# Kernel tuning notes

Measured on AMD Instinct MI355X. Metric: run time of the kernel, lower is better.

Reference implementation:

```python
import jax, jax.numpy as jnp
import numpy as np

N = 50000
E = 800000
IN_DIM = 16
H = 128
L = 4
EDGE_DIM = 7
LN_EPS = 1e-5


def _linear_params(key, fan_in, fan_out):
    kw, kb = jax.random.split(key)
    w = jax.random.normal(kw, (fan_in, fan_out), jnp.float32) * 0.02
    b = jax.random.normal(kb, (fan_out,), jnp.float32) * 0.02
    return w, b


def setup_inputs() -> dict:
    key = jax.random.key(0)
    ks = jax.random.split(key, 20)
    x = jax.random.normal(ks[0], (N, IN_DIM), jnp.float32)
    pos = jax.random.uniform(ks[1], (N, 3), jnp.float32) * 10.0
    row = jax.random.randint(ks[2], (E,), 0, N, jnp.int32)
    # guarantee no self-loops so distance > 0 (radius_graph uses loop=False)
    off = jax.random.randint(ks[3], (E,), 1, N, jnp.int32)
    col = (row + off) % N
    edge_index = jnp.stack([row, col], axis=0)

    W_in, b_in = _linear_params(ks[4], IN_DIM, H)

    def stack_layers(kbase, fan_in, fan_out):
        ws, bs = [], []
        for l in range(L):
            w, b = _linear_params(jax.random.fold_in(kbase, l), fan_in, fan_out)
            ws.append(w); bs.append(b)
        return jnp.stack(ws), jnp.stack(bs)

    We1, be1 = stack_layers(ks[5], 2 * H + EDGE_DIM, H)
    We2, be2 = stack_layers(ks[6], H, H)
    We3, be3 = stack_layers(ks[7], H, H)
    Wn1, bn1 = stack_layers(ks[8], H + H, H)
    Wn2, bn2 = stack_layers(ks[9], H, H)
    Wn3, bn3 = stack_layers(ks[10], H, H)
    ln_g = jnp.ones((L, H), jnp.float32)
    ln_b = jnp.zeros((L, H), jnp.float32)

    return {
        'x': x, 'pos': pos, 'edge_index': edge_index,
        'W_in': W_in, 'b_in': b_in,
        'We1': We1, 'be1': be1, 'We2': We2, 'be2': be2, 'We3': We3, 'be3': be3,
        'Wn1': Wn1, 'bn1': bn1, 'Wn2': Wn2, 'bn2': bn2, 'Wn3': Wn3, 'bn3': bn3,
        'ln_g': ln_g, 'ln_b': ln_b,
    }


def reference(x, pos, edge_index, W_in, b_in, We1, be1, We2, be2, We3, be3,
              Wn1, bn1, Wn2, bn2, Wn3, bn3, ln_g, ln_b):
    n = x.shape[0]
    row, col = edge_index[0], edge_index[1]  # row=source, col=target (PyG)
    rel_pos = pos[col] - pos[row]                       # (E, 3)
    dist = jnp.linalg.norm(rel_pos, axis=1, keepdims=True)  # (E, 1)
    edge_attr = jnp.concatenate([rel_pos, dist], axis=1)    # (E, 4)

    h = x @ W_in + b_in  # (N, H)
    num_layers = We1.shape[0]
    for l in range(num_layers):
        mom = h[:, 3:6]
        rel_mom = mom[col] - mom[row]                        # (E, 3)
        ea = jnp.concatenate([edge_attr, rel_mom], axis=1)   # (E, 7)
        # PyG: x_i = x[target=col], x_j = x[source=row]; EdgeMLP concats [h_i, h_j, ea]
        m = jnp.concatenate([h[col], h[row], ea], axis=1)    # (E, 2H+7)
        m = jax.nn.relu(m @ We1[l] + be1[l])
        m = jax.nn.relu(m @ We2[l] + be2[l])
        m = m @ We3[l] + be3[l]                              # (E, H)
        agg = jax.ops.segment_sum(m, col, num_segments=n)    # scatter-add to targets
        u = jnp.concatenate([h, agg], axis=1)                # (N, 2H)
        u = jax.nn.relu(u @ Wn1[l] + bn1[l])
        u = jax.nn.relu(u @ Wn2[l] + bn2[l])
        u = u @ Wn3[l] + bn3[l]                              # (N, H)
        h = h + u
        mean = jnp.mean(h, axis=-1, keepdims=True)
        var = jnp.mean(jnp.square(h - mean), axis=-1, keepdims=True)
        h = (h - mean) * jax.lax.rsqrt(var + LN_EPS) * ln_g[l] + ln_b[l]
    return h
```

## Files before the change

kernel.cpp:

```cpp
#include <hip/hip_runtime.h>
#include <stdint.h>

#define NN 50000
#define NE 800000
#define HD 128
#define NL 4
#define NM 64
#define EB 128
#define SCH ((NN + 1023) / 1024)

typedef __bf16 bf16x8 __attribute__((ext_vector_type(8)));
typedef __bf16 bf16x4 __attribute__((ext_vector_type(4)));
typedef float  f32x4  __attribute__((ext_vector_type(4)));

__device__ __forceinline__ f32x4 mfma16(bf16x8 a, bf16x8 b, f32x4 c) {
  return __builtin_amdgcn_mfma_f32_16x16x32_bf16(a, b, c, 0, 0, 0);
}

template<int MT, int NT>
__device__ __forceinline__ void zero_acc(f32x4 (&acc)[MT][NT]) {
#pragma unroll
  for (int i = 0; i < MT; ++i)
#pragma unroll
    for (int j = 0; j < NT; ++j) acc[i][j] = f32x4{0.f, 0.f, 0.f, 0.f};
}

template<int MT, int NT, int KS>
__device__ __forceinline__ void gemm_chunk(const __bf16* A, int sa,
    const __bf16* __restrict__ Bt, int Krow, int k0,
    int m_off, int n_off, int lane, f32x4 (&acc)[MT][NT])
{
  const int arow = lane & 15;
  const int quad = lane >> 4;
  bf16x8 b[KS][NT];
#pragma unroll
  for (int ks = 0; ks < KS; ++ks)
#pragma unroll
    for (int nt = 0; nt < NT; ++nt)
      b[ks][nt] = *reinterpret_cast<const bf16x8*>(
          Bt + (size_t)(n_off + nt * 16 + arow) * Krow + k0 + ks * 32 + quad * 8);
#pragma unroll
  for (int ks = 0; ks < KS; ++ks) {
    const int k = k0 + ks * 32 + quad * 8;
    bf16x8 a[MT];
#pragma unroll
    for (int mt = 0; mt < MT; ++mt)
      a[mt] = *reinterpret_cast<const bf16x8*>(A + (m_off + mt * 16 + arow) * sa + k);
#pragma unroll
    for (int mt = 0; mt < MT; ++mt)
#pragma unroll
      for (int nt = 0; nt < NT; ++nt)
        acc[mt][nt] = mfma16(a[mt], b[ks][nt], acc[mt][nt]);
  }
}

template<int MT, int NT, bool RELU>
__device__ __forceinline__ void store_tile(__bf16* O, int so,
    const float* __restrict__ bias, int m_off, int n_off, int lane,
    f32x4 (&acc)[MT][NT])
{
  const int quad = lane >> 4;
  const int cl = lane & 15;
#pragma unroll
  for (int nt = 0; nt < NT; ++nt) {
    const int col = n_off + nt * 16 + cl;
    const float bv = bias[col];
#pragma unroll
    for (int mt = 0; mt < MT; ++mt)
#pragma unroll
      for (int r = 0; r < 4; ++r) {
        const int row = m_off + mt * 16 + quad * 4 + r;
        float v = acc[mt][nt][r] + bv;
        if (RELU) v = fmaxf(v, 0.f);
        O[row * so + col] = (__bf16)v;
      }
  }
}

__global__ void prep_w(const float* __restrict__ W, __bf16* __restrict__ Wt,
                       int K0, int Kp) {
  int idx = blockIdx.x * 256 + threadIdx.x;
  int total = NL * HD * Kp;
  if (idx >= total) return;
  int l = idx / (HD * Kp);
  int rem = idx - l * HD * Kp;
  int n = rem / Kp;
  int k = rem - n * Kp;
  float v = (k < K0) ? W[((size_t)l * K0 + k) * HD + n] : 0.f;
  Wt[idx] = (__bf16)v;
}

__global__ void prep_pqw(const float* __restrict__ We1,
                         __bf16* __restrict__ Wtopt, __bf16* __restrict__ Wbott) {
  int idx = blockIdx.x * 256 + threadIdx.x;
  if (idx >= NL * HD * HD) return;
  int l = idx / (HD * HD);
  int rem = idx - l * HD * HD;
  int n = rem >> 7;
  int k = rem & 127;
  const float* W = We1 + (size_t)l * 263 * HD;
  float extra = (k >= 3 && k < 6) ? W[(260 + k - 3) * HD + n] : 0.f;
  Wtopt[idx] = (__bf16)(W[k * HD + n] + extra);
  Wbott[idx] = (__bf16)(W[(128 + k) * HD + n] - extra);
}

__global__ void h0_kernel(const float* __restrict__ x, const float* __restrict__ W,
                          const float* __restrict__ b, float* __restrict__ H32,
                          __bf16* __restrict__ HB) {
  int idx = blockIdx.x * 256 + threadIdx.x;
  if (idx >= NN * HD) return;
  int node = idx >> 7, j = idx & 127;
  const float* xr = x + node * 16;
  float s = b[j];
#pragma unroll
  for (int k = 0; k < 16; ++k) s += xr[k] * W[k * HD + j];
  H32[idx] = s;
  HB[idx] = (__bf16)s;
}

__global__ void hist_kernel(const int* __restrict__ ei, int* __restrict__ cnt) {
  int e = blockIdx.x * 256 + threadIdx.x;
  if (e < NE) atomicAdd(&cnt[ei[NE + e]], 1);
}

__global__ void scan_kernel(const int* __restrict__ cnt, int* __restrict__ cur) {
  __shared__ int wsum[16];
  const int t = threadIdx.x;
  const int lane = t & 63, wid = t >> 6;
  const int base = t * SCH;
  int s = 0;
  for (int k = 0; k < SCH; ++k) {
    int i = base + k;
    if (i < NN) s += cnt[i];
  }
  int incl = s;
#pragma unroll
  for (int off = 1; off < 64; off <<= 1) {
    int u = __shfl_up(incl, off, 64);
    if (lane >= off) incl += u;
  }
  if (lane == 63) wsum[wid] = incl;
  __syncthreads();
  int woff = 0;
  for (int k = 0; k < wid; ++k) woff += wsum[k];
  int run = woff + incl - s;
  for (int k = 0; k < SCH; ++k) {
    int i = base + k;
    if (i < NN) { cur[i] = run; run += cnt[i]; }
  }
}

__global__ void scatter_kernel(const int* __restrict__ ei, int* __restrict__ cur,
                               const float* __restrict__ pos,
                               int* __restrict__ ROWS, int* __restrict__ COLS,
                               __bf16* __restrict__ DSTb) {
  int e = blockIdx.x * 256 + threadIdx.x;
  if (e < NE) {
    int r = ei[e], c = ei[NE + e];
    int p = atomicAdd(&cur[c], 1);
    ROWS[p] = r;
    COLS[p] = c;
    float dx = pos[c * 3 + 0] - pos[r * 3 + 0];
    float dy = pos[c * 3 + 1] - pos[r * 3 + 1];
    float dz = pos[c * 3 + 2] - pos[r * 3 + 2];
    DSTb[p] = (__bf16)sqrtf(dx * dx + dy * dy + dz * dz);
  }
}

__global__ __launch_bounds__(256, 4) void pq_kernel(
    const __bf16* __restrict__ HB, const float* __restrict__ pos,
    const __bf16* __restrict__ Wtopt, const __bf16* __restrict__ Wbott,
    const float* __restrict__ W4xyz,
    const float* __restrict__ be1,
    __bf16* __restrict__ PB, __bf16* __restrict__ QB)
{
  __shared__ __bf16 SP[64 * 136];
  __shared__ __bf16 SQ[64 * 136];
  const int t = threadIdx.x;
  const int w = t >> 6, lane = t & 63;
  const int g = w & 1;
  const int half = w >> 1;
  const int base = blockIdx.x * 64;
  const int rbase = base + half * 32;
  const int arow = lane & 15, quad = lane >> 4, cl = lane & 15;

  const __bf16* Wt = g ? Wbott : Wtopt;
  __bf16* S = (g ? SQ : SP) + half * 32 * 136;

  f32x4 acc[2][8];
  zero_acc(acc);
#pragma unroll
  for (int ks = 0; ks < 4; ++ks) {
    const int k = ks * 32 + quad * 8;
    bf16x8 b[8];
#pragma unroll
    for (int nt = 0; nt < 8; ++nt)
      b[nt] = *reinterpret_cast<const bf16x8*>(Wt + (size_t)(nt * 16 + arow) * HD + k);
    bf16x8 a[2];
#pragma unroll
    for (int mt = 0; mt < 2; ++mt) {
      int row = rbase + mt * 16 + arow;
      if (row >= NN) row = NN - 1;
      a[mt] = *reinterpret_cast<const bf16x8*>(HB + (size_t)row * HD + k);
    }
#pragma unroll
    for (int mt = 0; mt < 2; ++mt)
#pragma unroll
      for (int nt = 0; nt < 8; ++nt)
        acc[mt][nt] = mfma16(a[mt], b[nt], acc[mt][nt]);
  }
  float px[2][4], py[2][4], pz[2][4];
#pragma unroll
  for (int mt = 0; mt < 2; ++mt)
#pragma unroll
    for (int r = 0; r < 4; ++r) {
      int row = rbase + mt * 16 + quad * 4 + r;
      if (row >= NN) row = NN - 1;
      px[mt][r] = pos[row * 3 + 0];
      py[mt][r] = pos[row * 3 + 1];
      pz[mt][r] = pos[row * 3 + 2];
    }
#pragma unroll
  for (int nt = 0; nt < 8; ++nt) {
    const int col = nt * 16 + cl;
    const float w0 = W4xyz[col], w1 = W4xyz[HD + col], w2 = W4xyz[2 * HD + col];
    const float bb = g ? 0.f : be1[col];
#pragma unroll
    for (int mt = 0; mt < 2; ++mt)
#pragma unroll
      for (int r = 0; r < 4; ++r) {
        const int row = mt * 16 + quad * 4 + r;
        float dot = px[mt][r] * w0 + py[mt][r] * w1 + pz[mt][r] * w2;
        float v = acc[mt][nt][r] + (g ? -dot : dot) + bb;
        S[row * 136 + col] = (__bf16)v;
      }
  }
  __syncthreads();
#pragma unroll
  for (int u = 0; u < 4; ++u) {
    const int idx = u * 256 + t;
    const int row = idx >> 4, ch = idx & 15;
    const int node = base + row;
    if (node < NN) {
      *reinterpret_cast<uint4*>(PB + (size_t)node * HD + ch * 8) =
          *reinterpret_cast<const uint4*>(SP + row * 136 + ch * 8);
      *reinterpret_cast<uint4*>(QB + (size_t)node * HD + ch * 8) =
          *reinterpret_cast<const uint4*>(SQ + row * 136 + ch * 8);
    }
  }
}

__global__ __launch_bounds__(512, 4) void edge_kernel(
    const __bf16* __restrict__ PB, const __bf16* __restrict__ QB,
    const __bf16* __restrict__ DSTb,
    const int* __restrict__ ROWS, const int* __restrict__ COLS,
    const float* __restrict__ w4d,
    const __bf16* __restrict__ We2t, const __bf16* __restrict__ We3t,
    const float* __restrict__ be2, const float* __restrict__ be3,
    float* __restrict__ AGG)
{
  __shared__ __bf16 S1[EB * 136];
  __shared__ __bf16 S2[EB * 136];
  __shared__ float w4ds[HD], be2s[HD], be3s[HD];
  __shared__ int colS[EB];
  __shared__ unsigned long long bmaskS[EB / 64];
  const int t = threadIdx.x;

  const int nwg = gridDim.x;
  const int q = nwg >> 3, r8 = nwg & 7;
  const int xcd = blockIdx.x & 7, idx8 = blockIdx.x >> 3;
  const int bswz = (xcd < r8 ? xcd * (q + 1) : r8 * (q + 1) + (xcd - r8) * q) + idx8;
  const int base = bswz * EB;

  if (t < HD) { w4ds[t] = w4d[t]; be2s[t] = be2[t]; be3s[t] = be3[t]; }
  if (t < EB) colS[t] = COLS[base + t];
  __syncthreads();

  if (t < EB) {
    int d = (t == EB - 1) || (colS[t + 1] != colS[t]);
    unsigned long long bm = __ballot(d);
    if ((t & 63) == 0) bmaskS[t >> 6] = bm;
  }

  {
    const int i = t >> 2, cg = t & 3;
    const int p = base + i;
    const int c = colS[i];
    const int r = ROWS[p];
    const float dist = (float)DSTb[p];
    const __bf16* Prow = PB + (size_t)c * HD;
    const __bf16* Qrow = QB + (size_t)r * HD;
#pragma unroll
    for (int u = 0; u < 4; ++u) {
      const int ch = cg * 4 + u;
      bf16x8 pv = *reinterpret_cast<const bf16x8*>(Prow + ch * 8);
      bf16x8 qv = *reinterpret_cast<const bf16x8*>(Qrow + ch * 8);
      bf16x8 o;
#pragma unroll
      for (int j = 0; j < 8; ++j) {
        const int col = ch * 8 + j;
        float f = (float)pv[j] + (float)qv[j] + dist * w4ds[col];
        o[j] = (__bf16)fmaxf(f, 0.f);
      }
      *reinterpret_cast<bf16x8*>(S1 + i * 136 + ch * 8) = o;
    }
  }
  __syncthreads();

  const int w = t >> 6, lane = t & 63;
  const int m_off = (w >> 2) * 64, n_off = (w & 3) * 32;
  const int arow = lane & 15, quad = lane >> 4, cl = lane & 15;

  f32x4 acc[4][2];
#pragma unroll
  for (int g = 0; g < 2; ++g) {
    const __bf16* Wt = g ? We3t : We2t;
    const float* bs = g ? be3s : be2s;
    const __bf16* Sin  = g ? S2 : S1;
    __bf16* Sout = g ? S1 : S2;

    bf16x8 b[4][2];
#pragma unroll
    for (int ks = 0; ks < 4; ++ks)
#pragma unroll
      for (int nt = 0; nt < 2; ++nt)
        b[ks][nt] = *reinterpret_cast<const bf16x8*>(
            Wt + (size_t)(n_off + nt * 16 + arow) * HD + ks * 32 + quad * 8);

    zero_acc(acc);
#pragma unroll
    for (int ks = 0; ks < 4; ++ks) {
      const int k = ks * 32 + quad * 8;
      bf16x8 a[4];
#pragma unroll
      for (int mt = 0; mt < 4; ++mt)
        a[mt] = *reinterpret_cast<const bf16x8*>(Sin + (m_off + mt * 16 + arow) * 136 + k);
#pragma unroll
      for (int mt = 0; mt < 4; ++mt)
#pragma unroll
        for (int nt = 0; nt < 2; ++nt)
          acc[mt][nt] = mfma16(a[mt], b[ks][nt], acc[mt][nt]);
    }
#pragma unroll
    for (int nt = 0; nt < 2; ++nt) {
      const int col = n_off + nt * 16 + cl;
      const float bv = bs[col];
#pragma unroll
      for (int mt = 0; mt < 4; ++mt)
#pragma unroll
        for (int r = 0; r < 4; ++r) {
          const int row = m_off + mt * 16 + quad * 4 + r;
          float v = acc[mt][nt][r] + bv;
          if (!g) v = fmaxf(v, 0.f);
          Sout[row * 136 + col] = (__bf16)v;
        }
    }
    __syncthreads();
  }

  {
    const int j = t & 127, qtr = t >> 7;
    const int i0 = qtr * 32;
    unsigned int m = (unsigned int)(bmaskS[qtr >> 1] >> ((qtr & 1) * 32));
    m |= 0x80000000u;
    float s = 0.f;
    for (int r = 0; r < 32; ++r) {
      const int i = i0 + r;
      s += (float)S1[i * 136 + j];
      if ((m >> r) & 1u) {
        atomicAdd(&AGG[(size_t)colS[i] * HD + j], s);
        s = 0.f;
      }
    }
  }
}

__global__ __launch_bounds__(256, 4) void node_kernel(
    const __bf16* __restrict__ HBin, float* __restrict__ AGG,
    const __bf16* __restrict__ Wn1t, const __bf16* __restrict__ Wn2t,
    const __bf16* __restrict__ Wn3t,
    const float* __restrict__ bn1, const float* __restrict__ bn2,
    const float* __restrict__ bn3,
    const float* __restrict__ lng, const float* __restrict__ lnb,
    float* __restrict__ H32, __bf16* __restrict__ HBout,
    float* __restrict__ dout)
{
  __shared__ float SB[NM * 136];
  __shared__ float ps[NM][2], psq[NM][2];
  __shared__ float mean_s[NM], rstd_s[NM];
  __bf16* B16 = reinterpret_cast<__bf16*>(SB);
  const int t = threadIdx.x;
  const int base = blockIdx.x * NM;

  {
    const int i0 = t >> 4, s = t & 15;
#pragma unroll
    for (int g = 0; g < NM / 16; ++g) {
      const int i = g * 16 + i0;
      const int node = base + i;
      uint4 v = make_uint4(0, 0, 0, 0);
      if (node < NN) v = *(reinterpret_cast<const uint4*>(HBin + (size_t)node * HD) + s);
      *reinterpret_cast<uint4*>(&B16[i * 264 + s * 8]) = v;
    }
  }
  for (int idx = t; idx < NM * 32; idx += 256) {
    const int i = idx >> 5, c4 = idx & 31;
    const int node = base + i;
    float4 v = make_float4(0.f, 0.f, 0.f, 0.f);
    if (node < NN) {
      float4* ap = reinterpret_cast<float4*>(AGG + (size_t)node * HD + c4 * 4);
      v = *ap;
      *ap = make_float4(0.f, 0.f, 0.f, 0.f);
    }
    __bf16* d = &B16[i * 264 + HD + c4 * 4];
    d[0] = (__bf16)v.x; d[1] = (__bf16)v.y; d[2] = (__bf16)v.z; d[3] = (__bf16)v.w;
  }
  __syncthreads();

  const int w = t >> 6, lane = t & 63;
  const int m_off = (w >> 1) * 32, n_off = (w & 1) * 64;
  f32x4 acc[2][4];
  __bf16* reg0 = B16;
  __bf16* reg1 = B16 + NM * 136;

  zero_acc(acc);
  gemm_chunk<2, 4, 4>(B16, 264, Wn1t, 256, 0,   m_off, n_off, lane, acc);
  gemm_chunk<2, 4, 4>(B16, 264, Wn1t, 256, 128, m_off, n_off, lane, acc);
  __syncthreads();
  store_tile<2, 4, true>(reg0, 136, bn1, m_off, n_off, lane, acc);
  __syncthreads();
  zero_acc(acc);
  gemm_chunk<2, 4, 4>(reg0, 136, Wn2t, 128, 0, m_off, n_off, lane, acc);
  store_tile<2, 4, true>(reg1, 136, bn2, m_off, n_off, lane, acc);
  __syncthreads();
  zero_acc(acc);
  gemm_chunk<2, 4, 4>(reg1, 136, Wn3t, 128, 0, m_off, n_off, lane, acc);
  __syncthreads();

  {
    const int quad = lane >> 4, cl = lane & 15;
#pragma unroll
    for (int nt = 0; nt < 4; ++nt) {
      const int col = n_off + nt * 16 + cl;
      const float bv = bn3[col];
#pragma unroll
      for (int mt = 0; mt < 2; ++mt)
#pragma unroll
        for (int r = 0; r < 4; ++r) {
          const int row = m_off + mt * 16 + quad * 4 + r;
          const int node = base + row;
          float hv = (node < NN) ? H32[(size_t)node * HD + col] : 0.f;
          SB[row * 136 + col] = hv + acc[mt][nt][r] + bv;
        }
    }
  }
  __syncthreads();
  if (t < 128) {
    const int r = t >> 1, hh = t & 1;
    float s = 0.f, sq = 0.f;
    for (int j = hh * 64; j < hh * 64 + 64; ++j) {
      float v = SB[r * 136 + j];
      s += v; sq += v * v;
    }
    ps[r][hh] = s; psq[r][hh] = sq;
  }
  __syncthreads();
  if (t < NM) {
    float s = ps[t][0] + ps[t][1];
    float sq = psq[t][0] + psq[t][1];
    float mean = s * (1.f / HD);
    float var = sq * (1.f / HD) - mean * mean;
    mean_s[t] = mean;
    rstd_s[t] = rsqrtf(var + 1e-5f);
  }
  __syncthreads();
  for (int idx = t; idx < NM * HD; idx += 256) {
    const int r = idx >> 7, j = idx & 127;
    const int node = base + r;
    if (node < NN) {
      float v = (SB[r * 136 + j] - mean_s[r]) * rstd_s[r] * lng[j] + lnb[j];
      H32[(size_t)node * HD + j] = v;
      HBout[(size_t)node * HD + j] = (__bf16)v;
      if (dout) dout[(size_t)node * HD + j] = v;
    }
  }
}

extern "C" void kernel_launch(void* const* d_in, const int* in_sizes, int n_in,
                              void* d_out, int out_size, void* d_ws, size_t ws_size,
                              hipStream_t stream)
{
  const float* x    = (const float*)d_in[0];
  const float* pos  = (const float*)d_in[1];
  const int*   ei   = (const int*)d_in[2];
  const float* W_in = (const float*)d_in[3];
  const float* b_in = (const float*)d_in[4];
  const float* We1  = (const float*)d_in[5];
  const float* be1  = (const float*)d_in[6];
  const float* We2  = (const float*)d_in[7];
  const float* be2  = (const float*)d_in[8];
  const float* We3  = (const float*)d_in[9];
  const float* be3  = (const float*)d_in[10];
  const float* Wn1  = (const float*)d_in[11];
  const float* bn1  = (const float*)d_in[12];
  const float* Wn2  = (const float*)d_in[13];
  const float* bn2  = (const float*)d_in[14];
  const float* Wn3  = (const float*)d_in[15];
  const float* bn3  = (const float*)d_in[16];
  const float* lng  = (const float*)d_in[17];
  const float* lnb  = (const float*)d_in[18];
  float* out = (float*)d_out;

  char* ws = (char*)d_ws;
  size_t off = 0;
  auto alloc = [&](size_t bytes) -> char* {
    char* p = ws + off;
    off += (bytes + 255) & ~(size_t)255;
    return p;
  };
  __bf16* Wtopt = (__bf16*)alloc((size_t)NL * HD * HD * 2);
  __bf16* Wbott = (__bf16*)alloc((size_t)NL * HD * HD * 2);
  __bf16* We2t = (__bf16*)alloc((size_t)NL * HD * HD * 2);
  __bf16* We3t = (__bf16*)alloc((size_t)NL * HD * HD * 2);
  __bf16* Wn1t = (__bf16*)alloc((size_t)NL * HD * 256 * 2);
  __bf16* Wn2t = (__bf16*)alloc((size_t)NL * HD * HD * 2);
  __bf16* Wn3t = (__bf16*)alloc((size_t)NL * HD * HD * 2);
  __bf16* DSTb = (__bf16*)alloc((size_t)NE * 2);
  float*  H32  = (float*) alloc((size_t)NN * HD * 4);
  __bf16* HB   = (__bf16*)alloc((size_t)NN * HD * 2);
  __bf16* PB   = (__bf16*)alloc((size_t)NN * HD * 2);
  __bf16* QB   = (__bf16*)alloc((size_t)NN * HD * 2);
  float*  AGG  = (float*) alloc((size_t)NN * HD * 4);
  int*    CNT  = (int*)   alloc((size_t)NN * 4);
  int*    CUR  = (int*)   alloc((size_t)NN * 4);
  int*    ROWS = (int*)   alloc((size_t)NE * 4);
  int*    COLS = (int*)   alloc((size_t)NE * 4);

  hipMemsetAsync(CNT, 0, (size_t)NN * 4, stream);
  hipMemsetAsync(AGG, 0, (size_t)NN * HD * 4, stream);
  prep_pqw<<<(NL * HD * HD + 255) / 256, 256, 0, stream>>>(We1, Wtopt, Wbott);
  prep_w<<<(NL * HD * HD + 255) / 256, 256, 0, stream>>>(We2, We2t, 128, 128);
  prep_w<<<(NL * HD * HD + 255) / 256, 256, 0, stream>>>(We3, We3t, 128, 128);
  prep_w<<<(NL * HD * 256 + 255) / 256, 256, 0, stream>>>(Wn1, Wn1t, 256, 256);
  prep_w<<<(NL * HD * HD + 255) / 256, 256, 0, stream>>>(Wn2, Wn2t, 128, 128);
  prep_w<<<(NL * HD * HD + 255) / 256, 256, 0, stream>>>(Wn3, Wn3t, 128, 128);
  h0_kernel<<<(NN * HD + 255) / 256, 256, 0, stream>>>(x, W_in, b_in, H32, HB);
  hist_kernel<<<(NE + 255) / 256, 256, 0, stream>>>(ei, CNT);
  scan_kernel<<<1, 1024, 0, stream>>>(CNT, CUR);
  scatter_kernel<<<(NE + 255) / 256, 256, 0, stream>>>(ei, CUR, pos, ROWS, COLS, DSTb);

  const int pq_blocks = (NN + 63) / 64;
  for (int l = 0; l < NL; ++l) {
    const float* We1l = We1 + (size_t)l * 263 * HD;
    pq_kernel<<<pq_blocks, 256, 0, stream>>>(HB, pos,
        Wtopt + (size_t)l * HD * HD, Wbott + (size_t)l * HD * HD,
        We1l + 256 * HD,
        be1 + l * HD, PB, QB);
    edge_kernel<<<NE / EB, 512, 0, stream>>>(PB, QB, DSTb, ROWS, COLS,
        We1l + 259 * HD,
        We2t + (size_t)l * HD * HD, We3t + (size_t)l * HD * HD,
        be2 + l * HD, be3 + l * HD, AGG);
    node_kernel<<<(NN + NM - 1) / NM, 256, 0, stream>>>(HB, AGG,
        Wn1t + (size_t)l * HD * 256, Wn2t + (size_t)l * HD * HD,
        Wn3t + (size_t)l * HD * HD,
        bn1 + l * HD, bn2 + l * HD, bn3 + l * HD,
        lng + l * HD, lnb + l * HD,
        H32, HB, (l == NL - 1) ? out : nullptr);
  }
}
```

Baseline: 1.238 ms.

## Fuse next layer's P/Q projection into node kernel epilogue

The node kernel now computes the next layer's P and Q edge-MLP projections directly from the freshly normalized h held in shared memory, so the separate pq_kernel launch per layer is dropped; it runs once only for layer 0. This avoids re-reading HB from global memory and three kernel launches. HB writes are vectorized via shared memory and skipped on the last layer. The node kernel gains extra MFMA work, register pressure (vreg[32]) and syncs, which may reduce occupancy.

```diff
diff --git a/kernel.cpp b/kernel.cpp
--- a/kernel.cpp
+++ b/kernel.cpp
@@ -382,8 +382,12 @@
     const float* __restrict__ bn1, const float* __restrict__ bn2,
     const float* __restrict__ bn3,
     const float* __restrict__ lng, const float* __restrict__ lnb,
+    const __bf16* __restrict__ Wtop_nxt, const __bf16* __restrict__ Wbot_nxt,
+    const float* __restrict__ W4xyz_nxt, const float* __restrict__ be1_nxt,
+    const float* __restrict__ pos,
     float* __restrict__ H32, __bf16* __restrict__ HBout,
-    float* __restrict__ dout)
+    float* __restrict__ dout,
+    __bf16* __restrict__ PBout, __bf16* __restrict__ QBout)
 {
   __shared__ float SB[NM * 136];
   __shared__ float ps[NM][2], psq[NM][2];
@@ -419,6 +423,7 @@
 
   const int w = t >> 6, lane = t & 63;
   const int m_off = (w >> 1) * 32, n_off = (w & 1) * 64;
+  const int arow = lane & 15, quad = lane >> 4, cl = lane & 15;
   f32x4 acc[2][4];
   __bf16* reg0 = B16;
   __bf16* reg1 = B16 + NM * 136;
@@ -438,7 +443,6 @@
   __syncthreads();
 
   {
-    const int quad = lane >> 4, cl = lane & 15;
 #pragma unroll
     for (int nt = 0; nt < 4; ++nt) {
       const int col = n_off + nt * 16 + cl;
@@ -474,14 +478,95 @@
     rstd_s[t] = rsqrtf(var + 1e-5f);
   }
   __syncthreads();
-  for (int idx = t; idx < NM * HD; idx += 256) {
+
+  float vreg[32];
+#pragma unroll
+  for (int u = 0; u < 32; ++u) {
+    const int idx = u * 256 + t;
     const int r = idx >> 7, j = idx & 127;
     const int node = base + r;
+    float v = 0.f;
     if (node < NN) {
-      float v = (SB[r * 136 + j] - mean_s[r]) * rstd_s[r] * lng[j] + lnb[j];
+      v = (SB[r * 136 + j] - mean_s[r]) * rstd_s[r] * lng[j] + lnb[j];
       H32[(size_t)node * HD + j] = v;
-      HBout[(size_t)node * HD + j] = (__bf16)v;
       if (dout) dout[(size_t)node * HD + j] = v;
+    }
+    vreg[u] = v;
+  }
+  __syncthreads();
+#pragma unroll
+  for (int u = 0; u < 32; ++u) {
+    const int idx = u * 256 + t;
+    const int r = idx >> 7, j = idx & 127;
+    B16[r * 136 + j] = (__bf16)vreg[u];
+  }
+  __syncthreads();
+
+  if (HBout) {
+#pragma unroll
+    for (int u = 0; u < 4; ++u) {
+      const int idx = u * 256 + t;
+      const int r = idx >> 4, ch = idx & 15;
+      const int node = base + r;
+      if (node < NN)
+        *reinterpret_cast<uint4*>(HBout + (size_t)node * HD + ch * 8) =
+            *reinterpret_cast<const uint4*>(B16 + r * 136 + ch * 8);
+    }
+  }
+
+  if (PBout) {
+    __bf16* Sst = reg1;
+    float px[4], py[4], pz[4];
+#pragma unroll
+    for (int r = 0; r < 4; ++r) {
+      int row = base + w * 16 + quad * 4 + r;
+      if (row >= NN) row = NN - 1;
+      px[r] = pos[row * 3 + 0];
+      py[r] = pos[row * 3 + 1];
+      pz[r] = pos[row * 3 + 2];
+    }
+#pragma unroll
+    for (int g = 0; g < 2; ++g) {
+      const __bf16* Wt = g ? Wbot_nxt : Wtop_nxt;
+      f32x4 pacc[8];
+#pragma unroll
+      for (int n = 0; n < 8; ++n) pacc[n] = f32x4{0.f, 0.f, 0.f, 0.f};
+#pragma unroll
+      for (int ks = 0; ks < 4; ++ks) {
+        const int k = ks * 32 + quad * 8;
+        bf16x8 a = *reinterpret_cast<const bf16x8*>(B16 + (w * 16 + arow) * 136 + k);
+#pragma unroll
+        for (int nt = 0; nt < 8; ++nt) {
+          bf16x8 b = *reinterpret_cast<const bf16x8*>(
+              Wt + (size_t)(nt * 16 + arow) * HD + k);
+          pacc[nt] = mfma16(a, b, pacc[nt]);
+        }
+      }
+#pragma unroll
+      for (int nt = 0; nt < 8; ++nt) {
+        const int col = nt * 16 + cl;
+        const float w0 = W4xyz_nxt[col], w1 = W4xyz_nxt[HD + col],
+                    w2 = W4xyz_nxt[2 * HD + col];
+        const float bb = g ? 0.f : be1_nxt[col];
+#pragma unroll
+        for (int r = 0; r < 4; ++r) {
+          const int lr = w * 16 + quad * 4 + r;
+          float dot = px[r] * w0 + py[r] * w1 + pz[r] * w2;
+          Sst[lr * 136 + col] = (__bf16)(pacc[nt][r] + (g ? -dot : dot) + bb);
+        }
+      }
+      __syncthreads();
+      __bf16* O = g ? QBout : PBout;
+#pragma unroll
+      for (int u = 0; u < 4; ++u) {
+        const int idx = u * 256 + t;
+        const int r = idx >> 4, ch = idx & 15;
+        const int node = base + r;
+        if (node < NN)
+          *reinterpret_cast<uint4*>(O + (size_t)node * HD + ch * 8) =
+              *reinterpret_cast<const uint4*>(Sst + r * 136 + ch * 8);
+      }
+      __syncthreads();
     }
   }
 }
@@ -550,12 +635,13 @@
   scatter_kernel<<<(NE + 255) / 256, 256, 0, stream>>>(ei, CUR, pos, ROWS, COLS, DSTb);
 
   const int pq_blocks = (NN + 63) / 64;
+  pq_kernel<<<pq_blocks, 256, 0, stream>>>(HB, pos,
+      Wtopt, Wbott, We1 + 256 * HD, be1, PB, QB);
+
   for (int l = 0; l < NL; ++l) {
     const float* We1l = We1 + (size_t)l * 263 * HD;
-    pq_kernel<<<pq_blocks, 256, 0, stream>>>(HB, pos,
-        Wtopt + (size_t)l * HD * HD, Wbott + (size_t)l * HD * HD,
-        We1l + 256 * HD,
-        be1 + l * HD, PB, QB);
+    const bool last = (l == NL - 1);
+    const float* We1n = We1 + (size_t)(l + 1) * 263 * HD;
     edge_kernel<<<NE / EB, 512, 0, stream>>>(PB, QB, DSTb, ROWS, COLS,
         We1l + 259 * HD,
         We2t + (size_t)l * HD * HD, We3t + (size_t)l * HD * HD,
@@ -565,6 +651,14 @@
         Wn3t + (size_t)l * HD * HD,
         bn1 + l * HD, bn2 + l * HD, bn3 + l * HD,
         lng + l * HD, lnb + l * HD,
-        H32, HB, (l == NL - 1) ? out : nullptr);
-  }
-}
+        last ? nullptr : Wtopt + (size_t)(l + 1) * HD * HD,
+        last ? nullptr : Wbott + (size_t)(l + 1) * HD * HD,
+        last ? nullptr : We1n + 256 * HD,
+        last ? nullptr : be1 + (l + 1) * HD,
+        pos,
+        H32,
+        last ? nullptr : HB,
+        last ? out : nullptr,
+        last ? nullptr : PB, last ? nullptr : QB);
+  }
+}
```

Measured after the change: 1.242 ms. Within noise of the previous version (+0.3%).
